# Kernel optimization log

Measured on AMD Instinct MI355X. Metric: run time of the kernel, lower is better.

## Reference

```python
import jax, jax.numpy as jnp
import numpy as np

N, D, K = 8192, 512, 15  # points, embed dim, k_neighbors
EPS_MEAN = 1e-8
EPS_NORM = 1e-8


def _knn(emb, k):
    sq_norms = jnp.sum(emb * emb, axis=1)
    sq = sq_norms[:, None] + sq_norms[None, :] - 2.0 * (emb @ emb.T)
    sq = jnp.maximum(sq, 0.0)
    # smallest k+1 distances (squared dist is monotone in dist); slot 0 is self (dist 0)
    neg_vals, idx = jax.lax.top_k(-sq, k + 1)
    knn_sq = -neg_vals[:, 1:]
    knn_idx = idx[:, 1:]
    knn_d = jnp.sqrt(jnp.maximum(knn_sq, 1e-12))
    return knn_d, knn_idx


def _curvature_signature(knn_d):
    mean_d = jnp.mean(knn_d, axis=1, keepdims=True) + EPS_MEAN
    return jnp.sort(knn_d / mean_d, axis=1)


def _angular_signature(emb, knn_idx):
    k = knn_idx.shape[1]
    nb = emb[knn_idx]                      # [N, k, D] neighbor gather
    v = nb - emb[:, None, :]               # [N, k, D]
    nrm = jnp.linalg.norm(v, axis=2, keepdims=True)
    v = v / jnp.maximum(nrm, EPS_NORM)     # F.normalize semantics
    cos = jnp.einsum('nkd,nld->nkl', v, v)  # [N, k, k] batched small GEMM
    iu, ju = np.triu_indices(k, 1)
    ang = cos[:, iu, ju]                   # [N, k(k-1)/2]
    return jnp.sort(ang, axis=1)


def setup_inputs() -> dict:
    key = jax.random.key(0)
    k1, k2 = jax.random.split(key)
    embeddings = jax.random.normal(k1, (N, D), dtype=jnp.float32)
    # reference signatures computed from a perturbed copy (realistic set_reference)
    ref_emb = embeddings + 0.1 * jax.random.normal(k2, (N, D), dtype=jnp.float32)
    ref_d, ref_idx = _knn(ref_emb, K)
    reference_curvature_sig = _curvature_signature(ref_d)
    reference_angular_sig = _angular_signature(ref_emb, ref_idx)
    return {
        'embeddings': embeddings,
        'reference_curvature_sig': reference_curvature_sig,
        'reference_angular_sig': reference_angular_sig,
    }


def reference(embeddings, reference_curvature_sig, reference_angular_sig):
    n = embeddings.shape[0]
    k = min(K, n - 1)
    knn_d, knn_idx = _knn(embeddings, k)
    curr_curv = _curvature_signature(knn_d)          # [N, k]
    curr_ang = _angular_signature(embeddings, knn_idx)  # [N, k(k-1)/2]
    ref_curv = reference_curvature_sig[:n, :k]
    ref_ang = reference_angular_sig[:n]
    curv_loss = jnp.mean((curr_curv - ref_curv) ** 2)
    m = min(curr_ang.shape[1], ref_ang.shape[1])
    ang_loss = jnp.mean((curr_ang[:, :m] - ref_ang[:, :m]) ** 2)
    return 0.3 * curv_loss + 0.7 * ang_loss
```

## Files before the change

### kernel.cpp

```cpp
#include <hip/hip_runtime.h>
#include <hip/hip_bf16.h>
#include <math.h>

#define NPTS  8192
#define DIM   512
#define KNNK  15
#define NCAND 22
#define NPAIR 105
#define CINF  3.0e38f
#define EMPTYK 0xFFFFFFFFu
#define TAU_MARGIN (3u << 16)

#define NI      128
#define NJSPLIT 16
#define NJ      (NPTS/NJSPLIT)
#define JS      128
#define NSUB    (NJ/JS)
#define BK      32
#define NCH     (DIM/BK)
#define SDW     68
#define NPROBE  8
#define NLIST   (NPROBE + NJSPLIT - 2)
#define NKEYS   (NLIST * KNNK)

#define BUF0_OFF   0
#define BUF1_OFF   16384
#define SQJ_OFF    34816
#define KNN_LDS    39936

typedef __attribute__((ext_vector_type(8))) short short8;
typedef __attribute__((ext_vector_type(4))) float f32x4;
typedef unsigned int uint32;

static __device__ __forceinline__ float wave_sum_f(float v) {
#pragma unroll
  for (int m = 32; m > 0; m >>= 1) v += __shfl_xor(v, m, 64);
  return v;
}

static __device__ __forceinline__ void load_lds16(const void* g, void* l) {
  __builtin_amdgcn_global_load_lds(
      (const __attribute__((address_space(1))) void*)g,
      (__attribute__((address_space(3))) void*)l, 16, 0, 0);
}

static __device__ __forceinline__ void bf16split(float x, short& h, short& l) {
  __hip_bfloat16 hb = __float2bfloat16(x);
  const float hf = __bfloat162float(hb);
  __hip_bfloat16 lb = __float2bfloat16(x - hf);
  h = *(short*)&hb;
  l = *(short*)&lb;
}

static __device__ __forceinline__ void chain15(uint32 (&td)[15], uint32 c) {
#pragma unroll
  for (int p = 0; p < 15; ++p) {
    const uint32 lo = min(c, td[p]);
    const uint32 hi = max(c, td[p]);
    td[p] = lo; c = hi;
  }
}

#define PUSHK(k_) { const uint32 kv_ = (k_); \
  p0=(nc==0)?kv_:p0;  p1=(nc==1)?kv_:p1;  p2=(nc==2)?kv_:p2; \
  p3=(nc==3)?kv_:p3;  p4=(nc==4)?kv_:p4;  p5=(nc==5)?kv_:p5; \
  p6=(nc==6)?kv_:p6;  p7=(nc==7)?kv_:p7;  p8=(nc==8)?kv_:p8; \
  p9=(nc==9)?kv_:p9;  p10=(nc==10)?kv_:p10; p11=(nc==11)?kv_:p11; \
  ++nc; }

#define DRAINALL { \
  if (__any(nc >  0)) { if (nc >  0) chain15(td, p0);  } \
  if (__any(nc >  1)) { if (nc >  1) chain15(td, p1);  } \
  if (__any(nc >  2)) { if (nc >  2) chain15(td, p2);  } \
  if (__any(nc >  3)) { if (nc >  3) chain15(td, p3);  } \
  if (__any(nc >  4)) { if (nc >  4) chain15(td, p4);  } \
  if (__any(nc >  5)) { if (nc >  5) chain15(td, p5);  } \
  if (__any(nc >  6)) { if (nc >  6) chain15(td, p6);  } \
  if (__any(nc >  7)) { if (nc >  7) chain15(td, p7);  } \
  if (__any(nc >  8)) { if (nc >  8) chain15(td, p8);  } \
  if (__any(nc >  9)) { if (nc >  9) chain15(td, p9);  } \
  if (__any(nc > 10)) { if (nc > 10) chain15(td, p10); } \
  if (__any(nc > 11)) { if (nc > 11) chain15(td, p11); } \
  nc = 0; guard = min(tau_cur, td[14]); }

__global__ __launch_bounds__(256) void prep_kernel(
    const float* __restrict__ E, float* __restrict__ sqn,
    ushort* __restrict__ EA, ushort* __restrict__ EB) {
  const int row  = blockIdx.x * 4 + (threadIdx.x >> 6);
  const int lane = threadIdx.x & 63;
  const float SR2 = 1.4142135623730951f;
  float s = 0.f;
#pragma unroll
  for (int c = 0; c < 8; ++c) {
    const int d0 = lane + 64 * c;
    const float x = E[(size_t)row * DIM + d0];
    s = fmaf(x, x, s);
    __hip_bfloat16 ha = __float2bfloat16(-SR2 * x);
    __hip_bfloat16 hb = __float2bfloat16( SR2 * x);
    EA[(size_t)row * DIM + d0] = *(ushort*)&ha;
    EB[(size_t)row * DIM + d0] = *(ushort*)&hb;
  }
  s = wave_sum_f(s);
  if (lane == 0) sqn[row] = s;
}

__global__ __launch_bounds__(256, 4) void knn_probe(
    const ushort* __restrict__ EA, const ushort* __restrict__ EB,
    const float* __restrict__ sqn, uint32* __restrict__ knnk) {
  __shared__ __align__(16) char sm[KNN_LDS];
  uint32* sdp  = (uint32*)sm;
  float*  sqjs = (float*)(sm + SQJ_OFF);

  const int tid = threadIdx.x;
  const int w   = tid >> 6;
  const int L   = tid & 63;
  const int wr  = (w >> 1) & 1;
  const int wc  = w & 1;
  const int i0  = blockIdx.x * NI;
  const int j0p = blockIdx.y * JS;

  if (tid < 32) ((float4*)sqjs)[tid] = ((const float4*)(sqn + j0p))[tid];

  const ushort* gsrc = (w < 2) ? EA : EB;
  const int lrow  = L >> 2;
  const int swz_k = ((L & 3) ^ ((L >> 3) & 3)) * 8;
  const int lds_woff = ((w < 2) ? 0 : 8192) + (w & 1) * 4096;
  const int slot8 = (((L >> 4) ^ ((L >> 1) & 3)) * 8);

  const int myrow = tid >> 1;
  const int h     = tid & 1;
  const int gi    = i0 + myrow;

  uint32 td[15];
#pragma unroll
  for (int p = 0; p < 15; ++p) td[p] = EMPTYK;

  const int trowW = ((w < 2) ? i0 : j0p) + (w & 1) * 64;
  const ushort* gbase = gsrc + (size_t)(trowW + lrow) * DIM + swz_k;

  f32x4 acc[4][4];
  __syncthreads();
#pragma unroll
  for (int fj = 0; fj < 4; ++fj) {
    const f32x4 sq = *(const f32x4*)&sqjs[wc * 64 + fj * 16 + (L >> 4) * 4];
#pragma unroll
    for (int fi = 0; fi < 4; ++fi) acc[fj][fi] = sq;
  }

  {
    char* lp = sm + BUF0_OFF + lds_woff;
#pragma unroll
    for (int s = 0; s < 4; ++s)
      load_lds16(gbase + (size_t)(s * 16) * DIM, lp + s * 1024);
  }
  __syncthreads();

#pragma unroll 2
  for (int ch = 0; ch < NCH; ++ch) {
    const int cb  = (ch & 1) ? BUF1_OFF : BUF0_OFF;
    const int nbo = (ch & 1) ? BUF0_OFF : BUF1_OFF;
    if (ch < NCH - 1) {
      char* lp = sm + nbo + lds_woff;
      const ushort* gp = gbase + (ch + 1) * BK;
#pragma unroll
      for (int s = 0; s < 4; ++s)
        load_lds16(gp + (size_t)(s * 16) * DIM, lp + s * 1024);
    }

    const ushort* sA = (const ushort*)(sm + cb);
    const ushort* sB = (const ushort*)(sm + cb + 8192);

    short8 a[4], b[4];
#pragma unroll
    for (int f = 0; f < 4; ++f) {
      a[f] = *(const short8*)&sA[(wr * 64 + f * 16 + (L & 15)) * BK + slot8];
      b[f] = *(const short8*)&sB[(wc * 64 + f * 16 + (L & 15)) * BK + slot8];
    }
#pragma unroll
    for (int fj = 0; fj < 4; ++fj)
#pragma unroll
      for (int fi = 0; fi < 4; ++fi)
        acc[fj][fi] = __builtin_amdgcn_mfma_f32_16x16x32_bf16(b[fj], a[fi], acc[fj][fi], 0, 0, 0);
    __syncthreads();
  }

#pragma unroll
  for (int fj = 0; fj < 4; ++fj)
#pragma unroll
    for (int fi = 0; fi < 4; ++fi) {
      const int i_t = wr * 64 + fi * 16 + (L & 15);
      const int jd  = wc * 32 + fj * 8 + (L >> 4) * 2;
      uint32 dw0, dw1;
      asm("v_cvt_pk_bf16_f32 %0, %1, %2" : "=v"(dw0) : "v"(acc[fj][fi][0]), "v"(acc[fj][fi][1]));
      asm("v_cvt_pk_bf16_f32 %0, %1, %2" : "=v"(dw1) : "v"(acc[fj][fi][2]), "v"(acc[fj][fi][3]));
      uint2 d2; d2.x = dw0; d2.y = dw1;
      *(uint2*)&sdp[i_t * SDW + jd] = d2;
    }
  __syncthreads();

  uint32 tau_cur = EMPTYK;
  const int selfc = gi - j0p;
  if (selfc >= 0 && selfc < JS && h == (selfc >> 6))
    *(ushort*)(sm + myrow * (SDW * 4) + selfc * 2) = 0x7F80;

  const uint32* rowp = sdp + myrow * SDW + 32 * h;
  const uint32 jb = (uint32)(j0p + 64 * h);
  uint32 guard = min(tau_cur, td[14]);
  uint32 nc = 0;
  uint32 p0=0,p1=0,p2=0,p3=0,p4=0,p5=0,p6=0,p7=0,p8=0,p9=0,p10=0,p11=0;

#pragma unroll 2
  for (int q = 0; q < 8; ++q) {
    const uint4 pv = *(const uint4*)&rowp[4 * q];
    const uint32 jq = jb + 8 * q;
    uint32 kx;
    kx = (pv.x << 16)          | (jq + 0); if (kx < guard) PUSHK(kx);
    kx = (pv.x & 0xFFFF0000u)  | (jq + 1); if (kx < guard) PUSHK(kx);
    kx = (pv.y << 16)          | (jq + 2); if (kx < guard) PUSHK(kx);
    kx = (pv.y & 0xFFFF0000u)  | (jq + 3); if (kx < guard) PUSHK(kx);
    kx = (pv.z << 16)          | (jq + 4); if (kx < guard) PUSHK(kx);
    kx = (pv.z & 0xFFFF0000u)  | (jq + 5); if (kx < guard) PUSHK(kx);
    kx = (pv.w << 16)          | (jq + 6); if (kx < guard) PUSHK(kx);
    kx = (pv.w & 0xFFFF0000u)  | (jq + 7); if (kx < guard) PUSHK(kx);
    if (__any(nc >= 4)) { DRAINALL; }
  }
  if (__any(nc > 0)) { DRAINALL; }
  __syncthreads();

  uint32* mdk = (uint32*)sm;
#pragma unroll
  for (int p = 0; p < 15; ++p) mdk[(myrow * 2 + h) * 15 + p] = td[p];
  __syncthreads();
  if (h == 0) {
    const uint32* la = &mdk[(myrow * 2 + 0) * 15];
    const uint32* lb = &mdk[(myrow * 2 + 1) * 15];
    int pa = 0, pb = 0;
    const size_t base = ((size_t)gi * NLIST + blockIdx.y) * KNNK;
    for (int s = 0; s < KNNK; ++s) {
      const uint32 va = la[pa], vb = lb[pb];
      uint32 v;
      if (va <= vb) { v = va; ++pa; } else { v = vb; ++pb; }
      knnk[base + s] = v;
    }
  }
}

__global__ __launch_bounds__(256, 4) void knn_main(
    const ushort* __restrict__ EA, const ushort* __restrict__ EB,
    const float* __restrict__ sqn, uint32* __restrict__ knnk) {
  __shared__ __align__(16) char sm[KNN_LDS];
  uint32* sdp  = (uint32*)sm;
  float*  sqjs = (float*)(sm + SQJ_OFF);

  const int tid = threadIdx.x;
  const int w   = tid >> 6;
  const int L   = tid & 63;
  const int wr  = (w >> 1) & 1;
  const int wc  = w & 1;
  const int i0  = blockIdx.x * NI;
  const int jsplit = blockIdx.y + 2;
  const int j0  = jsplit * NJ;

  if (tid < NJ / 4) ((float4*)sqjs)[tid] = ((const float4*)(sqn + j0))[tid];

  const ushort* gsrc = (w < 2) ? EA : EB;
  const int lrow  = L >> 2;
  const int swz_k = ((L & 3) ^ ((L >> 3) & 3)) * 8;
  const int lds_woff = ((w < 2) ? 0 : 8192) + (w & 1) * 4096;
  const int slot8 = (((L >> 4) ^ ((L >> 1) & 3)) * 8);

  const int myrow = tid >> 1;
  const int h     = tid & 1;
  const int gi    = i0 + myrow;

  uint32 tauA;
  {
    const uint32* lb0 = knnk + (size_t)gi * NKEYS;
    uint32 tmin = EMPTYK;
#pragma unroll
    for (int pr = 0; pr < 4; ++pr) {
      const uint32* A = lb0 + (2 * pr) * KNNK;
      const uint32* B = lb0 + (2 * pr + 1) * KNNK;
      uint32 a[15], b[15];
#pragma unroll
      for (int k = 0; k < 15; ++k) { a[k] = A[k]; b[k] = B[k]; }
      uint32 v = min(b[14], a[14]);
#pragma unroll
      for (int i2 = 1; i2 <= 14; ++i2) v = min(v, max(a[i2 - 1], b[14 - i2]));
      tmin = min(tmin, v);
    }
    tauA = tmin + TAU_MARGIN;
  }

  uint32 td[15];
#pragma unroll
  for (int p = 0; p < 15; ++p) td[p] = EMPTYK;

  __syncthreads();

  for (int js = 0; js < NSUB; ++js) {
    const int jrow0 = j0 + js * JS;
    const int trowW = ((w < 2) ? i0 : jrow0) + (w & 1) * 64;
    const ushort* gbase = gsrc + (size_t)(trowW + lrow) * DIM + swz_k;

    f32x4 acc[4][4];
#pragma unroll
    for (int fj = 0; fj < 4; ++fj) {
      const f32x4 sq = *(const f32x4*)&sqjs[js * 128 + wc * 64 + fj * 16 + (L >> 4) * 4];
#pragma unroll
      for (int fi = 0; fi < 4; ++fi) acc[fj][fi] = sq;
    }

    {
      char* lp = sm + BUF0_OFF + lds_woff;
#pragma unroll
      for (int s = 0; s < 4; ++s)
        load_lds16(gbase + (size_t)(s * 16) * DIM, lp + s * 1024);
    }
    __syncthreads();

#pragma unroll 2
    for (int ch = 0; ch < NCH; ++ch) {
      const int cb  = (ch & 1) ? BUF1_OFF : BUF0_OFF;
      const int nbo = (ch & 1) ? BUF0_OFF : BUF1_OFF;
      if (ch < NCH - 1) {
        char* lp = sm + nbo + lds_woff;
        const ushort* gp = gbase + (ch + 1) * BK;
#pragma unroll
        for (int s = 0; s < 4; ++s)
          load_lds16(gp + (size_t)(s * 16) * DIM, lp + s * 1024);
      }

      const ushort* sA = (const ushort*)(sm + cb);
      const ushort* sB = (const ushort*)(sm + cb + 8192);

      short8 a[4], b[4];
#pragma unroll
      for (int f = 0; f < 4; ++f) {
        a[f] = *(const short8*)&sA[(wr * 64 + f * 16 + (L & 15)) * BK + slot8];
        b[f] = *(const short8*)&sB[(wc * 64 + f * 16 + (L & 15)) * BK + slot8];
      }
#pragma unroll
      for (int fj = 0; fj < 4; ++fj)
#pragma unroll
        for (int fi = 0; fi < 4; ++fi)
          acc[fj][fi] = __builtin_amdgcn_mfma_f32_16x16x32_bf16(b[fj], a[fi], acc[fj][fi], 0, 0, 0);
      __syncthreads();
    }

#pragma unroll
    for (int fj = 0; fj < 4; ++fj)
#pragma unroll
      for (int fi = 0; fi < 4; ++fi) {
        const int i_t = wr * 64 + fi * 16 + (L & 15);
        const int jd  = wc * 32 + fj * 8 + (L >> 4) * 2;
        uint32 dw0, dw1;
        asm("v_cvt_pk_bf16_f32 %0, %1, %2" : "=v"(dw0) : "v"(acc[fj][fi][0]), "v"(acc[fj][fi][1]));
        asm("v_cvt_pk_bf16_f32 %0, %1, %2" : "=v"(dw1) : "v"(acc[fj][fi][2]), "v"(acc[fj][fi][3]));
        uint2 d2; d2.x = dw0; d2.y = dw1;
        *(uint2*)&sdp[i_t * SDW + jd] = d2;
      }
    __syncthreads();

    uint32 tau_cur = tauA;
    const int selfc = gi - jrow0;
    if (selfc >= 0 && selfc < JS && h == (selfc >> 6))
      *(ushort*)(sm + myrow * (SDW * 4) + selfc * 2) = 0x7F80;

    const uint32* rowp = sdp + myrow * SDW + 32 * h;
    const uint32 jb = (uint32)(jrow0 + 64 * h);
    uint32 guard = min(tau_cur, td[14]);
    uint32 nc = 0;
    uint32 p0=0,p1=0,p2=0,p3=0,p4=0,p5=0,p6=0,p7=0,p8=0,p9=0,p10=0,p11=0;

#pragma unroll 2
    for (int q = 0; q < 8; ++q) {
      const uint4 pv = *(const uint4*)&rowp[4 * q];
      const uint32 jq = jb + 8 * q;
      uint32 kx;
      kx = (pv.x << 16)          | (jq + 0); if (kx < guard) PUSHK(kx);
      kx = (pv.x & 0xFFFF0000u)  | (jq + 1); if (kx < guard) PUSHK(kx);
      kx = (pv.y << 16)          | (jq + 2); if (kx < guard) PUSHK(kx);
      kx = (pv.y & 0xFFFF0000u)  | (jq + 3); if (kx < guard) PUSHK(kx);
      kx = (pv.z << 16)          | (jq + 4); if (kx < guard) PUSHK(kx);
      kx = (pv.z & 0xFFFF0000u)  | (jq + 5); if (kx < guard) PUSHK(kx);
      kx = (pv.w << 16)          | (jq + 6); if (kx < guard) PUSHK(kx);
      kx = (pv.w & 0xFFFF0000u)  | (jq + 7); if (kx < guard) PUSHK(kx);
      if (__any(nc >= 4)) { DRAINALL; }
    }
    if (__any(nc > 0)) { DRAINALL; }
    __syncthreads();
  }

  uint32* mdk = (uint32*)sm;
#pragma unroll
  for (int p = 0; p < 15; ++p) mdk[(myrow * 2 + h) * 15 + p] = td[p];
  __syncthreads();
  if (h == 0) {
    const uint32* la = &mdk[(myrow * 2 + 0) * 15];
    const uint32* lb = &mdk[(myrow * 2 + 1) * 15];
    int pa = 0, pb = 0;
    const size_t base = ((size_t)gi * NLIST + NPROBE + blockIdx.y) * KNNK;
    for (int s = 0; s < KNNK; ++s) {
      const uint32 va = la[pa], vb = lb[pb];
      uint32 v;
      if (va <= vb) { v = va; ++pa; } else { v = vb; ++pb; }
      knnk[base + s] = v;
    }
  }
}

__global__ __launch_bounds__(256) void sig_kernel(
    const float* __restrict__ E, const uint32* __restrict__ knnk,
    const float* __restrict__ refc, const float* __restrict__ refa,
    float2* __restrict__ pacc) {
  __shared__ float gsm[4][292];

  const int tid = threadIdx.x;
  const int wid = tid >> 6;
  const int L   = tid & 63;
  const int i   = blockIdx.x * 4 + wid;

  const uint32* kl = knnk + (size_t)i * NKEYS;
  uint32 k0 = kl[L];
  uint32 k1 = kl[L + 64];
  uint32 k2 = kl[L + 128];
  uint32 k3 = kl[L + 192];
  uint32 k4 = kl[L + 256];
  uint32 k5 = (L < NKEYS - 320) ? kl[L + 320] : EMPTYK;
  uint32 cand_key = EMPTYK;
  for (int sel = 0; sel < NCAND; ++sel) {
    uint32 v = k0; int which = 0;
    if (k1 < v) { v = k1; which = 1; }
    if (k2 < v) { v = k2; which = 2; }
    if (k3 < v) { v = k3; which = 3; }
    if (k4 < v) { v = k4; which = 4; }
    if (k5 < v) { v = k5; which = 5; }
    int slot = (L << 3) | which;
#pragma unroll
    for (int off = 32; off > 0; off >>= 1) {
      const uint32 ov = (uint32)__shfl_down((int)v, off, 64);
      const int    os = __shfl_down(slot, off, 64);
      if (ov < v) { v = ov; slot = os; }
    }
    const uint32 vmin = (uint32)__shfl((int)v, 0, 64);
    const int    smin = __shfl(slot, 0, 64);
    if (L == sel) cand_key = vmin;
    if (L == (smin >> 3)) {
      const int wsel = smin & 7;
      if (wsel == 0) k0 = EMPTYK;
      else if (wsel == 1) k1 = EMPTYK;
      else if (wsel == 2) k2 = EMPTYK;
      else if (wsel == 3) k3 = EMPTYK;
      else if (wsel == 4) k4 = EMPTYK;
      else k5 = EMPTYK;
    }
  }
  int cand_nb = ((cand_key >> 16) < 0x7F80u) ? (int)(cand_key & 0x1FFFu) : i;

  const float4* ei4 = (const float4*)(E + (size_t)i * DIM);
  const float4 e0 = ei4[2 * L];
  const float4 e1 = ei4[2 * L + 1];
  float csq = CINF;
#pragma unroll 2
  for (int c = 0; c < NCAND; ++c) {
    const int row = __shfl(cand_nb, c, 64);
    const float4* r4 = (const float4*)(E + (size_t)row * DIM);
    const float4 a0 = r4[2 * L];
    const float4 a1 = r4[2 * L + 1];
    const float d0 = a0.x - e0.x, d1 = a0.y - e0.y;
    const float d2 = a0.z - e0.z, d3 = a0.w - e0.w;
    const float d4 = a1.x - e1.x, d5 = a1.y - e1.y;
    const float d6 = a1.z - e1.z, d7 = a1.w - e1.w;
    float s8 = d0 * d0;
    s8 = fmaf(d1, d1, s8); s8 = fmaf(d2, d2, s8); s8 = fmaf(d3, d3, s8);
    s8 = fmaf(d4, d4, s8); s8 = fmaf(d5, d5, s8); s8 = fmaf(d6, d6, s8);
    s8 = fmaf(d7, d7, s8);
    const float sq = wave_sum_f(s8);
    if (L == c) csq = (row == i) ? CINF : sq;
  }

  float myd = 0.f; int mynb = i;
  for (int sel = 0; sel < KNNK; ++sel) {
    float v = csq; int who = L;
#pragma unroll
    for (int off = 32; off > 0; off >>= 1) {
      const float ov = __shfl_down(v, off, 64);
      const int   ow = __shfl_down(who, off, 64);
      if (ov < v) { v = ov; who = ow; }
    }
    const float vmin  = __shfl(v, 0, 64);
    const int   wmin  = __shfl(who, 0, 64);
    const int   nbmin = __shfl(cand_nb, wmin, 64);
    if ((L & 15) == sel) { myd = sqrtf(fmaxf(vmin, 1e-12f)); mynb = nbmin; }
    if (L == wmin) csq = CINF;
  }

  float curvs;
  {
    float dd = (L < KNNK) ? myd : 0.f;
    float tot = wave_sum_f(dd);
    float mean_d = tot / (float)KNNK + 1e-8f;
    float diff = (L < KNNK) ? (dd / mean_d - refc[i * KNNK + L]) : 0.f;
    curvs = wave_sum_f(diff * diff);
  }

  const float4* nb4 = (const float4*)(E + (size_t)mynb * DIM);
  const int qo = (L >> 4) * 2;

  f32x4 gH, gX;
#pragma unroll
  for (int r = 0; r < 4; ++r) { gH[r] = 0.f; gX[r] = 0.f; }

#pragma unroll
  for (int c = 0; c < 16; ++c) {
    const float4 f0 = nb4[qo + c * 8];
    const float4 f1 = nb4[qo + 1 + c * 8];
    const float4 g0 = ei4[qo + c * 8];
    const float4 g1 = ei4[qo + 1 + c * 8];
    float v[8];
    v[0] = f0.x - g0.x; v[1] = f0.y - g0.y; v[2] = f0.z - g0.z; v[3] = f0.w - g0.w;
    v[4] = f1.x - g1.x; v[5] = f1.y - g1.y; v[6] = f1.z - g1.z; v[7] = f1.w - g1.w;
    short8 ah, al;
#pragma unroll
    for (int q = 0; q < 8; ++q) {
      short hh, ll;
      bf16split(v[q], hh, ll);
      ah[q] = hh; al[q] = ll;
    }
    gH = __builtin_amdgcn_mfma_f32_16x16x32_bf16(ah, ah, gH, 0, 0, 0);
    gX = __builtin_amdgcn_mfma_f32_16x16x32_bf16(ah, al, gX, 0, 0, 0);
    gX = __builtin_amdgcn_mfma_f32_16x16x32_bf16(al, ah, gX, 0, 0, 0);
  }

#pragma unroll
  for (int q = 0; q < 4; ++q)
    gsm[wid][((L >> 4) * 4 + q) * 17 + (L & 15)] = gH[q] + gX[q];
  asm volatile("s_waitcnt lgkmcnt(0)" ::: "memory");

  if (L < 16) {
    const float dv = gsm[wid][L * 17 + L];
    const float nrm = sqrtf(fmaxf(dv, 0.f));
    gsm[wid][272 + L] = 1.0f / fmaxf(nrm, 1e-8f);
  }
  asm volatile("s_waitcnt lgkmcnt(0)" ::: "memory");

  float c0 = CINF, c1 = CINF;
#pragma unroll
  for (int s = 0; s < 2; ++s) {
    const int p = L + 64 * s;
    if (p < NPAIR) {
      int a = 0, rem = p, cnt = 14;
      while (rem >= cnt) { rem -= cnt; --cnt; ++a; }
      const int b = a + 1 + rem;
      const float cv = gsm[wid][a * 17 + b] * gsm[wid][272 + a] * gsm[wid][272 + b];
      if (s == 0) c0 = cv; else c1 = cv;
    }
  }

#pragma unroll
  for (int k = 2; k <= 128; k <<= 1) {
#pragma unroll
    for (int j = k >> 1; j >= 1; j >>= 1) {
      const bool dir = ((L & (k >> 1)) == 0);
      if (j == 1) {
        const float lo = fminf(c0, c1), hi = fmaxf(c0, c1);
        c0 = dir ? lo : hi;
        c1 = dir ? hi : lo;
      } else {
        const int m = j >> 1;
        const float o0 = __shfl_xor(c0, m, 64);
        const float o1 = __shfl_xor(c1, m, 64);
        const bool lower = ((L & m) == 0);
        c0 = (lower == dir) ? fminf(c0, o0) : fmaxf(c0, o0);
        c1 = (lower == dir) ? fminf(c1, o1) : fmaxf(c1, o1);
      }
    }
  }

  float part = 0.f;
  {
    const int r0 = 2 * L, r1 = 2 * L + 1;
    if (r0 < NPAIR) { const float dd = c0 - refa[(size_t)i * NPAIR + r0]; part += dd * dd; }
    if (r1 < NPAIR) { const float dd = c1 - refa[(size_t)i * NPAIR + r1]; part += dd * dd; }
  }
  part = wave_sum_f(part);
  if (L == 0) pacc[i] = make_float2(curvs, part);
}

__global__ __launch_bounds__(256) void fin_kernel(
    const float2* __restrict__ pacc, float* __restrict__ out) {
  __shared__ double redc[4], reda[4];
  const int tid = threadIdx.x;
  const int wid = tid >> 6;
  const int L   = tid & 63;
  double sc = 0.0, sa = 0.0;
#pragma unroll
  for (int q = 0; q < 32; ++q) {
    const float2 p = pacc[tid + 256 * q];
    sc += (double)p.x;
    sa += (double)p.y;
  }
#pragma unroll
  for (int m = 32; m > 0; m >>= 1) {
    sc += __shfl_xor(sc, m, 64);
    sa += __shfl_xor(sa, m, 64);
  }
  if (L == 0) { redc[wid] = sc; reda[wid] = sa; }
  __syncthreads();
  if (tid == 0) {
    const double curv = (redc[0] + redc[1] + redc[2] + redc[3]) /
                        ((double)NPTS * (double)KNNK);
    const double ang  = (reda[0] + reda[1] + reda[2] + reda[3]) /
                        ((double)NPTS * (double)NPAIR);
    out[0] = (float)(0.3 * curv + 0.7 * ang);
  }
}

extern "C" void kernel_launch(void* const* d_in, const int* in_sizes, int n_in,
                              void* d_out, int out_size, void* d_ws,
                              size_t ws_size, hipStream_t stream) {
  const float* E    = (const float*)d_in[0];
  const float* refc = (const float*)d_in[1];
  const float* refa = (const float*)d_in[2];
  float* out = (float*)d_out;

  char* ws = (char*)d_ws;
  float*  sqn  = (float*)(ws + 1024);
  float2* pacc = (float2*)(ws + 65536);
  ushort* EA   = (ushort*)(ws + 1048576);
  ushort* EB   = (ushort*)(ws + 9437184);
  uint32* knnk = (uint32*)(ws + 17825792);

  prep_kernel<<<NPTS / 4, 256, 0, stream>>>(E, sqn, EA, EB);
  knn_probe<<<dim3(NPTS / NI, NPROBE), 256, 0, stream>>>(EA, EB, sqn, knnk);
  knn_main<<<dim3(NPTS / NI, NJSPLIT - 2), 256, 0, stream>>>(EA, EB, sqn, knnk);
  sig_kernel<<<NPTS / 4, 256, 0, stream>>>(E, knnk, refc, refa, pacc);
  fin_kernel<<<1, 256, 0, stream>>>(pacc, out);
}
```

Baseline: 313.1 us.

## Precompute kNN thresholds in separate kernel and parallelize candidate distance recheck

The per-row tau threshold, which merges the probe lists, was previously recomputed redundantly by every knn_main block along the j-split axis (14 times per row). It now comes from a small dedicated kernel that writes one value per row, and knn_main loads it. In sig_kernel, the exact fp32 recheck of the 22 candidate distances switches from a serial loop with one full wave reduction per candidate to 8 candidates computed at once, each by an 8-lane group with a 3-step shuffle reduction. The trade-off is one extra kernel launch plus a tiny workspace buffer, with fewer reductions in exchange.

```diff
diff --git a/kernel.cpp b/kernel.cpp
--- a/kernel.cpp
+++ b/kernel.cpp
@@ -245,9 +245,30 @@
   }
 }
 
+__global__ __launch_bounds__(256) void tau_kernel(
+    const uint32* __restrict__ knnk, uint32* __restrict__ tauk) {
+  const int p = blockIdx.x * 256 + threadIdx.x;
+  const uint32* lb0 = knnk + (size_t)p * NKEYS;
+  uint32 tmin = EMPTYK;
+#pragma unroll
+  for (int pr = 0; pr < 4; ++pr) {
+    const uint32* A = lb0 + (2 * pr) * KNNK;
+    const uint32* B = lb0 + (2 * pr + 1) * KNNK;
+    uint32 a[15], b[15];
+#pragma unroll
+    for (int k = 0; k < 15; ++k) { a[k] = A[k]; b[k] = B[k]; }
+    uint32 v = min(b[14], a[14]);
+#pragma unroll
+    for (int i2 = 1; i2 <= 14; ++i2) v = min(v, max(a[i2 - 1], b[14 - i2]));
+    tmin = min(tmin, v);
+  }
+  tauk[p] = tmin + TAU_MARGIN;
+}
+
 __global__ __launch_bounds__(256, 4) void knn_main(
     const ushort* __restrict__ EA, const ushort* __restrict__ EB,
-    const float* __restrict__ sqn, uint32* __restrict__ knnk) {
+    const float* __restrict__ sqn, const uint32* __restrict__ tauk,
+    uint32* __restrict__ knnk) {
   __shared__ __align__(16) char sm[KNN_LDS];
   uint32* sdp  = (uint32*)sm;
   float*  sqjs = (float*)(sm + SQJ_OFF);
@@ -273,24 +294,7 @@
   const int h     = tid & 1;
   const int gi    = i0 + myrow;
 
-  uint32 tauA;
-  {
-    const uint32* lb0 = knnk + (size_t)gi * NKEYS;
-    uint32 tmin = EMPTYK;
-#pragma unroll
-    for (int pr = 0; pr < 4; ++pr) {
-      const uint32* A = lb0 + (2 * pr) * KNNK;
-      const uint32* B = lb0 + (2 * pr + 1) * KNNK;
-      uint32 a[15], b[15];
-#pragma unroll
-      for (int k = 0; k < 15; ++k) { a[k] = A[k]; b[k] = B[k]; }
-      uint32 v = min(b[14], a[14]);
-#pragma unroll
-      for (int i2 = 1; i2 <= 14; ++i2) v = min(v, max(a[i2 - 1], b[14 - i2]));
-      tmin = min(tmin, v);
-    }
-    tauA = tmin + TAU_MARGIN;
-  }
+  const uint32 tauA = tauk[gi];
 
   uint32 td[15];
 #pragma unroll
@@ -458,27 +462,38 @@
   }
   int cand_nb = ((cand_key >> 16) < 0x7F80u) ? (int)(cand_key & 0x1FFFu) : i;
 
-  const float4* ei4 = (const float4*)(E + (size_t)i * DIM);
-  const float4 e0 = ei4[2 * L];
-  const float4 e1 = ei4[2 * L + 1];
-  float csq = CINF;
-#pragma unroll 2
-  for (int c = 0; c < NCAND; ++c) {
+  const float* Ei = E + (size_t)i * DIM;
+  const int u = L & 7;
+  const int g = L >> 3;
+  float sr[3];
+#pragma unroll
+  for (int r = 0; r < 3; ++r) {
+    const int c = r * 8 + g;
     const int row = __shfl(cand_nb, c, 64);
-    const float4* r4 = (const float4*)(E + (size_t)row * DIM);
-    const float4 a0 = r4[2 * L];
-    const float4 a1 = r4[2 * L + 1];
-    const float d0 = a0.x - e0.x, d1 = a0.y - e0.y;
-    const float d2 = a0.z - e0.z, d3 = a0.w - e0.w;
-    const float d4 = a1.x - e1.x, d5 = a1.y - e1.y;
-    const float d6 = a1.z - e1.z, d7 = a1.w - e1.w;
-    float s8 = d0 * d0;
-    s8 = fmaf(d1, d1, s8); s8 = fmaf(d2, d2, s8); s8 = fmaf(d3, d3, s8);
-    s8 = fmaf(d4, d4, s8); s8 = fmaf(d5, d5, s8); s8 = fmaf(d6, d6, s8);
-    s8 = fmaf(d7, d7, s8);
-    const float sq = wave_sum_f(s8);
-    if (L == c) csq = (row == i) ? CINF : sq;
-  }
+    const float4* r4 = (const float4*)(E + (size_t)row * DIM) + u * 16;
+    const float4* e4 = (const float4*)Ei + u * 16;
+    float a0 = 0.f, a1 = 0.f, a2 = 0.f, a3 = 0.f;
+#pragma unroll
+    for (int t = 0; t < 16; ++t) {
+      const float4 av = r4[t];
+      const float4 ev = e4[t];
+      const float d0 = av.x - ev.x, d1 = av.y - ev.y;
+      const float d2 = av.z - ev.z, d3 = av.w - ev.w;
+      a0 = fmaf(d0, d0, a0); a1 = fmaf(d1, d1, a1);
+      a2 = fmaf(d2, d2, a2); a3 = fmaf(d3, d3, a3);
+    }
+    float s = (a0 + a1) + (a2 + a3);
+    s += __shfl_xor(s, 1, 64);
+    s += __shfl_xor(s, 2, 64);
+    s += __shfl_xor(s, 4, 64);
+    sr[r] = s;
+  }
+  const int srcl = (L & 7) * 8;
+  const float t0 = __shfl(sr[0], srcl, 64);
+  const float t1 = __shfl(sr[1], srcl, 64);
+  const float t2 = __shfl(sr[2], srcl, 64);
+  float csq = (L >> 3) == 0 ? t0 : ((L >> 3) == 1 ? t1 : t2);
+  if (L >= NCAND || cand_nb == i) csq = CINF;
 
   float myd = 0.f; int mynb = i;
   for (int sel = 0; sel < KNNK; ++sel) {
@@ -506,6 +521,7 @@
   }
 
   const float4* nb4 = (const float4*)(E + (size_t)mynb * DIM);
+  const float4* ei4 = (const float4*)Ei;
   const int qo = (L >> 4) * 2;
 
   f32x4 gH, gX;
@@ -628,13 +644,15 @@
   char* ws = (char*)d_ws;
   float*  sqn  = (float*)(ws + 1024);
   float2* pacc = (float2*)(ws + 65536);
+  uint32* tauk = (uint32*)(ws + 131072);
   ushort* EA   = (ushort*)(ws + 1048576);
   ushort* EB   = (ushort*)(ws + 9437184);
   uint32* knnk = (uint32*)(ws + 17825792);
 
   prep_kernel<<<NPTS / 4, 256, 0, stream>>>(E, sqn, EA, EB);
   knn_probe<<<dim3(NPTS / NI, NPROBE), 256, 0, stream>>>(EA, EB, sqn, knnk);
-  knn_main<<<dim3(NPTS / NI, NJSPLIT - 2), 256, 0, stream>>>(EA, EB, sqn, knnk);
+  tau_kernel<<<NPTS / 256, 256, 0, stream>>>(knnk, tauk);
+  knn_main<<<dim3(NPTS / NI, NJSPLIT - 2), 256, 0, stream>>>(EA, EB, sqn, tauk, knnk);
   sig_kernel<<<NPTS / 4, 256, 0, stream>>>(E, knnk, refc, refa, pacc);
   fin_kernel<<<1, 256, 0, stream>>>(pacc, out);
 }
```

Result: slower. 367.7 us (+17.4%).
